# Performance work log

Hardware: AMD Instinct MI355X
Metric: run time of the kernel (lower is better)

The kernel has to match this reference:

```python
import jax, jax.numpy as jnp
import numpy as np

B, C, H, T = 256, 2048, 1024, 64  # batch, code_num, hidden_dim, max_len


def setup_inputs() -> dict:
    key = jax.random.key(0)
    ks = jax.random.split(key, 7)
    s_ih = 1.0 / np.sqrt(C)
    s_hh = 1.0 / np.sqrt(H)
    return {
        "noise": jax.random.normal(ks[0], (B, H), dtype=jnp.float32),
        "W_ih": jax.random.uniform(ks[1], (3 * H, C), jnp.float32, -s_ih, s_ih),
        "b_ih": jax.random.uniform(ks[2], (3 * H,), jnp.float32, -s_ih, s_ih),
        "W_hh": jax.random.uniform(ks[3], (3 * H, H), jnp.float32, -s_hh, s_hh),
        "b_hh": jax.random.uniform(ks[4], (3 * H,), jnp.float32, -s_hh, s_hh),
        "W_out": jax.random.uniform(ks[5], (C, H), jnp.float32, -s_hh, s_hh),
        "b_out": jax.random.uniform(ks[6], (C,), jnp.float32, -s_hh, s_hh),
        "max_len": T,
    }


def reference(noise, W_ih, b_ih, W_hh, b_hh, W_out, b_out, max_len):
    # initial codes = sigmoid(Linear(noise))
    codes0 = jax.nn.sigmoid(noise @ W_out.T + b_out)  # [B, C]
    h0 = jnp.zeros((noise.shape[0], W_hh.shape[1]), dtype=noise.dtype)  # [B, H]

    def step(carry, _):
        codes, h = carry
        gi = codes @ W_ih.T + b_ih           # [B, 3H]
        gh = h @ W_hh.T + b_hh               # [B, 3H]
        i_r, i_z, i_n = jnp.split(gi, 3, axis=-1)
        h_r, h_z, h_n = jnp.split(gh, 3, axis=-1)
        r = jax.nn.sigmoid(i_r + h_r)
        z = jax.nn.sigmoid(i_z + h_z)
        n = jnp.tanh(i_n + r * h_n)
        h_new = (1.0 - z) * n + z * h        # PyTorch GRUCell update
        logits = h_new @ W_out.T + b_out
        codes_new = jax.nn.sigmoid(logits)
        # sample at step t is codes BEFORE the cell; hidden is h AFTER
        return (codes_new, h_new), (codes, h_new)

    _, (samples, hiddens) = jax.lax.scan(step, (codes0, h0), None, length=max_len)
    samples = jnp.swapaxes(samples, 0, 1)  # [B, T, C]
    hiddens = jnp.swapaxes(hiddens, 0, 1)  # [B, T, H]
    return samples, hiddens
```

## Files before the change

### kernel.cpp

```cpp
#include <hip/hip_runtime.h>
#include <hip/hip_bf16.h>

#define BB 256
#define CC 2048
#define HD 1024
#define TT 64
#define H3 3072
#define NBLK 256
#define NGRP 8
#define GBLK 32
#define GROWS 32

typedef __attribute__((ext_vector_type(8)))  short bf16x8;
typedef __attribute__((ext_vector_type(4)))  float f32x4;
typedef __attribute__((ext_vector_type(16))) float f32x16;
typedef __attribute__((ext_vector_type(4)))  int   i32x4;

__device__ __forceinline__ float sigmoidf_(float x){ return 1.0f/(1.0f+__expf(-x)); }
__device__ __forceinline__ float tanhf_(float x){ float e=__expf(2.0f*x); return 1.0f - 2.0f/(e+1.0f); }
__device__ __forceinline__ unsigned short bfbits(float x){
  __hip_bfloat16 b = __float2bfloat16(x);
  return *reinterpret_cast<unsigned short*>(&b);
}
__device__ __forceinline__ void st_sys_bf16(__hip_bfloat16* p, float v){
  __hip_atomic_store((unsigned short*)p, bfbits(v), __ATOMIC_RELAXED, __HIP_MEMORY_SCOPE_SYSTEM);
}
__device__ __forceinline__ float ld_sys_bf16v(const __hip_bfloat16* p){
  unsigned short b = __hip_atomic_load((const unsigned short*)p, __ATOMIC_RELAXED, __HIP_MEMORY_SCOPE_SYSTEM);
  union { unsigned short u; __hip_bfloat16 h; } x; x.u = b;
  return __bfloat162float(x.h);
}
__device__ __forceinline__ i32x4 ld_sys16(const void* p){
  i32x4 r;
  asm volatile("global_load_dwordx4 %0, %1, off sc0 sc1"
               : "=v"(r) : "v"(p) : "memory");
  return r;
}
__device__ __forceinline__ void waitv0(){
  asm volatile("s_waitcnt vmcnt(0)" ::: "memory");
  __builtin_amdgcn_sched_barrier(0);
}
__device__ __forceinline__ void release_wb(){
  asm volatile("s_waitcnt vmcnt(0)\n\t"
               "buffer_wbl2 sc1\n\t"
               "s_waitcnt vmcnt(0)" ::: "memory");
}

__global__ void cvt_f32_bf16(const float* __restrict__ in, __hip_bfloat16* __restrict__ out, int n){
  int i = (blockIdx.x*blockDim.x + threadIdx.x)*4;
  int stride = gridDim.x*blockDim.x*4;
  for (; i < n; i += stride){
    float4 v = *reinterpret_cast<const float4*>(in + i);
    ushort4 s;
    s.x = bfbits(v.x); s.y = bfbits(v.y); s.z = bfbits(v.z); s.w = bfbits(v.w);
    *reinterpret_cast<ushort4*>(out + i) = s;
  }
}

#define MFMA32(a,b,c) __builtin_amdgcn_mfma_f32_32x32x16_bf16((a),(b),(c),0,0,0)

__global__ __launch_bounds__(1024, 4) void gru_persistent(
    const __hip_bfloat16* __restrict__ wih,
    const __hip_bfloat16* __restrict__ whh,
    const __hip_bfloat16* __restrict__ wout,
    const __hip_bfloat16* __restrict__ noise16,
    const float* __restrict__ bih,
    const float* __restrict__ bhh,
    const float* __restrict__ bout,
    float* __restrict__ samples,
    float* __restrict__ hiddens,
    __hip_bfloat16* cb0, __hip_bfloat16* cb1,
    __hip_bfloat16* hb0, __hip_bfloat16* hb1,
    unsigned* flagC, unsigned* flagH)
{
  __shared__ __align__(16) char actbuf[98304];
  __shared__ float ghbuf[3*4*256];

  const int tid  = threadIdx.x;
  const int lane = tid & 63;
  const int wid  = tid >> 6;
  const int g    = blockIdx.x >> 5;
  const int bsub = blockIdx.x & 31;
  const int lrow = lane & 31;
  const int lkg  = lane >> 5;

  auto signal = [&](unsigned* flags, unsigned gen){
    __syncthreads();
    if (tid == 0){
      release_wb();
      __hip_atomic_store(&flags[g*GBLK + bsub], gen, __ATOMIC_RELAXED, __HIP_MEMORY_SCOPE_SYSTEM);
    }
  };
  auto waitf = [&](unsigned* flags, unsigned gen){
    if (tid < GBLK){
      while (__hip_atomic_load(&flags[g*GBLK + tid], __ATOMIC_RELAXED, __HIP_MEMORY_SCOPE_SYSTEM) < gen)
        __builtin_amdgcn_s_sleep(2);
    }
    __syncthreads();
  };

  auto stage = [&](const __hip_bfloat16* src, int rowStride, int colBase){
    i32x4 r0, r1, r2, r3;
    {
      int s = tid;        int p = s>>6, l = s&63;
      r0 = ld_sys16(src + (size_t)(g*GROWS + (l&31))*rowStride + colBase + p*16 + (l>>5)*8);
    }{
      int s = tid+1024;   int p = s>>6, l = s&63;
      r1 = ld_sys16(src + (size_t)(g*GROWS + (l&31))*rowStride + colBase + p*16 + (l>>5)*8);
    }{
      int s = tid+2048;   int p = s>>6, l = s&63;
      r2 = ld_sys16(src + (size_t)(g*GROWS + (l&31))*rowStride + colBase + p*16 + (l>>5)*8);
    }{
      int s = tid+3072;   int p = s>>6, l = s&63;
      r3 = ld_sys16(src + (size_t)(g*GROWS + (l&31))*rowStride + colBase + p*16 + (l>>5)*8);
    }
    waitv0();
    { int s = tid;      *(i32x4*)(actbuf + (s>>6)*1024 + (s&63)*16) = r0; }
    { int s = tid+1024; *(i32x4*)(actbuf + (s>>6)*1024 + (s&63)*16) = r1; }
    { int s = tid+2048; *(i32x4*)(actbuf + (s>>6)*1024 + (s&63)*16) = r2; }
    { int s = tid+3072; *(i32x4*)(actbuf + (s>>6)*1024 + (s&63)*16) = r3; }
  };

  auto dumpAcc = [&](int slot, const f32x16& acc){
    char* base = actbuf + slot*4096 + lane*16;
#pragma unroll
    for (int q = 0; q < 4; q++){
      f32x4 v = { acc[q*4+0], acc[q*4+1], acc[q*4+2], acc[q*4+3] };
      *(f32x4*)(base + q*1024) = v;
    }
  };

  const f32x16 zacc = {0};

  auto phaseX = [&](const __hip_bfloat16* hsrc, __hip_bfloat16* codesDst, int t){
    stage(hsrc, HD, 0);
    __syncthreads();

    if (wid < 15){
      const int tile = wid / 3;
      const int ks   = wid % 3;
      const int fbeg = (ks == 0) ? 0 : (22 + 21*(ks-1));
      const int fend = (ks == 2) ? 64 : (22 + 21*ks);
      const __hip_bfloat16* wl;
      if (tile < 2) wl = wout + (size_t)(bsub*64 + tile*32 + lrow)*HD + lkg*8;
      else          wl = whh  + (size_t)((tile-2)*HD + bsub*32 + lrow)*HD + lkg*8;
      f32x16 acc = zacc;
#pragma unroll 8
      for (int f = fbeg; f < fend; f++){
        bf16x8 a = *(const bf16x8*)(actbuf + f*1024 + lane*16);
        bf16x8 b = *(const bf16x8*)(wl + f*16);
        acc = MFMA32(a, b, acc);
      }
      __syncthreads();
      dumpAcc(wid, acc);
    } else {
      __syncthreads();
    }
    __syncthreads();

    if (wid < 8){
      const int tile = wid >> 2, q = wid & 3;
      const int col  = bsub*64 + tile*32 + lrow;
      f32x4 s0 = *(const f32x4*)(actbuf + (tile*3+0)*4096 + q*1024 + lane*16);
      f32x4 s1 = *(const f32x4*)(actbuf + (tile*3+1)*4096 + q*1024 + lane*16);
      f32x4 s2 = *(const f32x4*)(actbuf + (tile*3+2)*4096 + q*1024 + lane*16);
      const float bo = bout[col];
#pragma unroll
      for (int j = 0; j < 4; j++){
        const int row  = j + 8*q + 4*lkg;
        const int brow = g*GROWS + row;
        float sv = sigmoidf_(s0[j] + s1[j] + s2[j] + bo);
        __builtin_nontemporal_store(sv, &samples[(size_t)brow*TT*CC + (size_t)t*CC + col]);
        st_sys_bf16(codesDst + (size_t)brow*CC + col, sv);
      }
    } else {
      for (int task = wid - 8; task < 12; task += 8){
        const int gt = task >> 2, q = task & 3;
        f32x4 r;
        if (t == 0){
          r = (f32x4){0.f,0.f,0.f,0.f};
        } else {
          f32x4 s0 = *(const f32x4*)(actbuf + ((2+gt)*3+0)*4096 + q*1024 + lane*16);
          f32x4 s1 = *(const f32x4*)(actbuf + ((2+gt)*3+1)*4096 + q*1024 + lane*16);
          f32x4 s2 = *(const f32x4*)(actbuf + ((2+gt)*3+2)*4096 + q*1024 + lane*16);
          r = (f32x4){ s0[0]+s1[0]+s2[0], s0[1]+s1[1]+s2[1],
                       s0[2]+s1[2]+s2[2], s0[3]+s1[3]+s2[3] };
        }
        *(f32x4*)&ghbuf[(gt*4+q)*256 + lane*4] = r;
      }
    }
  };

  auto phaseY = [&](const __hip_bfloat16* codesSrc, const __hip_bfloat16* hsrc,
                    __hip_bfloat16* hDst, int t){
    f32x16 acc = zacc;
    float hp[4]; float bI[3], bH[3];
    const int jcol = bsub*32 + lrow;

    stage(codesSrc, CC, 0);
    __syncthreads();
    if (wid < 12){
      const int gt = wid >> 2, ks = wid & 3;
      const __hip_bfloat16* wl = wih + (size_t)(gt*HD + bsub*32 + lrow)*CC + lkg*8;
#pragma unroll
      for (int i = 0; i < 16; i++){
        const int f = ks*16 + i;
        bf16x8 a = *(const bf16x8*)(actbuf + f*1024 + lane*16);
        bf16x8 b = *(const bf16x8*)(wl + f*16);
        acc = MFMA32(a, b, acc);
      }
    } else {
      const int q = wid - 12;
#pragma unroll
      for (int j = 0; j < 4; j++){
        const int row = j + 8*q + 4*lkg;
        hp[j] = (t == 0) ? 0.0f
              : ld_sys_bf16v(hsrc + (size_t)(g*GROWS + row)*HD + jcol);
      }
#pragma unroll
      for (int gt = 0; gt < 3; gt++){
        bI[gt] = bih[gt*HD + jcol];
        bH[gt] = bhh[gt*HD + jcol];
      }
    }
    __syncthreads();

    stage(codesSrc, CC, 1024);
    __syncthreads();
    if (wid < 12){
      const int gt = wid >> 2, ks = wid & 3;
      const __hip_bfloat16* wl = wih + (size_t)(gt*HD + bsub*32 + lrow)*CC + lkg*8;
#pragma unroll
      for (int i = 0; i < 16; i++){
        const int f = ks*16 + i;
        bf16x8 a = *(const bf16x8*)(actbuf + f*1024 + lane*16);
        bf16x8 b = *(const bf16x8*)(wl + 1024 + f*16);
        acc = MFMA32(a, b, acc);
      }
      __syncthreads();
      dumpAcc(wid, acc);
    } else {
      __syncthreads();
    }
    __syncthreads();

    if (wid >= 12){
      const int q = wid - 12;
      f32x4 gi[3], gh[3];
#pragma unroll
      for (int gt = 0; gt < 3; gt++){
        f32x4 s0 = *(const f32x4*)(actbuf + (gt*4+0)*4096 + q*1024 + lane*16);
        f32x4 s1 = *(const f32x4*)(actbuf + (gt*4+1)*4096 + q*1024 + lane*16);
        f32x4 s2 = *(const f32x4*)(actbuf + (gt*4+2)*4096 + q*1024 + lane*16);
        f32x4 s3 = *(const f32x4*)(actbuf + (gt*4+3)*4096 + q*1024 + lane*16);
        gi[gt] = (f32x4){ s0[0]+s1[0]+s2[0]+s3[0], s0[1]+s1[1]+s2[1]+s3[1],
                          s0[2]+s1[2]+s2[2]+s3[2], s0[3]+s1[3]+s2[3]+s3[3] };
        gh[gt] = *(const f32x4*)&ghbuf[(gt*4+q)*256 + lane*4];
      }
#pragma unroll
      for (int j = 0; j < 4; j++){
        const int row  = j + 8*q + 4*lkg;
        const int brow = g*GROWS + row;
        float r = sigmoidf_(gi[0][j] + gh[0][j] + bI[0] + bH[0]);
        float z = sigmoidf_(gi[1][j] + gh[1][j] + bI[1] + bH[1]);
        float n = tanhf_(gi[2][j] + bI[2] + r*(gh[2][j] + bH[2]));
        float hv = (1.0f - z)*n + z*hp[j];
        __builtin_nontemporal_store(hv, &hiddens[(size_t)brow*TT*HD + (size_t)t*HD + jcol]);
        st_sys_bf16(hDst + (size_t)brow*HD + jcol, hv);
      }
    }
  };

#pragma unroll 1
  for (int t = 0; t < TT; t++){
    const __hip_bfloat16* hcur = (t & 1) ? hb1 : hb0;
    __hip_bfloat16* codesCur   = (t & 1) ? cb1 : cb0;
    __hip_bfloat16* hnext      = (t & 1) ? hb0 : hb1;

    if (t > 0) waitf(flagH, (unsigned)t);
    phaseX((t == 0) ? noise16 : hcur, codesCur, t);
    signal(flagC, (unsigned)(t+1));

    waitf(flagC, (unsigned)(t+1));
    phaseY(codesCur, hcur, hnext, t);
    signal(flagH, (unsigned)(t+1));
  }
}

extern "C" void kernel_launch(void* const* d_in, const int* in_sizes, int n_in,
                              void* d_out, int out_size, void* d_ws, size_t ws_size,
                              hipStream_t stream) {
  const float* noise = (const float*)d_in[0];
  const float* W_ih  = (const float*)d_in[1];
  const float* b_ih  = (const float*)d_in[2];
  const float* W_hh  = (const float*)d_in[3];
  const float* b_hh  = (const float*)d_in[4];
  const float* W_out = (const float*)d_in[5];
  const float* b_out = (const float*)d_in[6];

  float* samples = (float*)d_out;
  float* hiddens = samples + (size_t)BB*TT*CC;

  char* w = (char*)d_ws;
  unsigned* flagC = (unsigned*)w;              w += 1024;
  unsigned* flagH = (unsigned*)w;              w += 1024;
  __hip_bfloat16* wih16 = (__hip_bfloat16*)w;  w += (size_t)H3*CC*2;
  __hip_bfloat16* whh16 = (__hip_bfloat16*)w;  w += (size_t)H3*HD*2;
  __hip_bfloat16* wout16= (__hip_bfloat16*)w;  w += (size_t)CC*HD*2;
  __hip_bfloat16* noise16=(__hip_bfloat16*)w;  w += (size_t)BB*HD*2;
  __hip_bfloat16* cb0   = (__hip_bfloat16*)w;  w += (size_t)BB*CC*2;
  __hip_bfloat16* cb1   = (__hip_bfloat16*)w;  w += (size_t)BB*CC*2;
  __hip_bfloat16* hb0   = (__hip_bfloat16*)w;  w += (size_t)BB*HD*2;
  __hip_bfloat16* hb1   = (__hip_bfloat16*)w;  w += (size_t)BB*HD*2;

  hipMemsetAsync(flagC, 0, 2048, stream);
  cvt_f32_bf16<<<2048, 256, 0, stream>>>(W_ih,  wih16,  H3*CC);
  cvt_f32_bf16<<<2048, 256, 0, stream>>>(W_hh,  whh16,  H3*HD);
  cvt_f32_bf16<<<1024, 256, 0, stream>>>(W_out, wout16, CC*HD);
  cvt_f32_bf16<<<256,  256, 0, stream>>>(noise, noise16, BB*HD);

  gru_persistent<<<NBLK, 1024, 0, stream>>>(
      wih16, whh16, wout16, noise16, b_ih, b_hh, b_out,
      samples, hiddens, cb0, cb1, hb0, hb1, flagC, flagH);
}
```

Measured before the change: 3.516 ms.

## Split persistent GRU across 512 blocks with 16-row groups and 16x16 MFMA

Doubles the persistent grid to 512 blocks, each owning 16 batch rows instead of 32, and switches from 32x32x16 to 16x16x32 bf16 MFMA tiles. Activations are staged in 512-column chunks through a double-buffered LDS buffer, with dedicated waves loading the next chunk while others compute. The previous hidden state is now kept in registers rather than reloaded from global memory. This cuts LDS use and per-block work to raise occupancy and parallelism, at the cost of more blocks in the flag-based cross-block barriers and reloading each weight tile for twice as many batch groups.

New measurement: 5.186 ms. +47.5%, slower.

```diff
diff --git a/kernel.cpp b/kernel.cpp
--- a/kernel.cpp
+++ b/kernel.cpp
@@ -6,14 +6,13 @@
 #define HD 1024
 #define TT 64
 #define H3 3072
-#define NBLK 256
-#define NGRP 8
+#define NBLK 512
+#define NGRP 16
 #define GBLK 32
-#define GROWS 32
+#define GROWS 16
 
 typedef __attribute__((ext_vector_type(8)))  short bf16x8;
 typedef __attribute__((ext_vector_type(4)))  float f32x4;
-typedef __attribute__((ext_vector_type(16))) float f32x16;
 typedef __attribute__((ext_vector_type(4)))  int   i32x4;
 
 __device__ __forceinline__ float sigmoidf_(float x){ return 1.0f/(1.0f+__expf(-x)); }
@@ -25,10 +24,8 @@
 __device__ __forceinline__ void st_sys_bf16(__hip_bfloat16* p, float v){
   __hip_atomic_store((unsigned short*)p, bfbits(v), __ATOMIC_RELAXED, __HIP_MEMORY_SCOPE_SYSTEM);
 }
-__device__ __forceinline__ float ld_sys_bf16v(const __hip_bfloat16* p){
-  unsigned short b = __hip_atomic_load((const unsigned short*)p, __ATOMIC_RELAXED, __HIP_MEMORY_SCOPE_SYSTEM);
-  union { unsigned short u; __hip_bfloat16 h; } x; x.u = b;
-  return __bfloat162float(x.h);
+__device__ __forceinline__ bf16x8 ldfrag(const __hip_bfloat16* p){
+  return *reinterpret_cast<const bf16x8*>(p);
 }
 __device__ __forceinline__ i32x4 ld_sys16(const void* p){
   i32x4 r;
@@ -57,9 +54,9 @@
   }
 }
 
-#define MFMA32(a,b,c) __builtin_amdgcn_mfma_f32_32x32x16_bf16((a),(b),(c),0,0,0)
-
-__global__ __launch_bounds__(1024, 4) void gru_persistent(
+#define MFMA16(a,b,c) __builtin_amdgcn_mfma_f32_16x16x32_bf16((a),(b),(c),0,0,0)
+
+__global__ __launch_bounds__(1024, 8) void gru_persistent(
     const __hip_bfloat16* __restrict__ wih,
     const __hip_bfloat16* __restrict__ whh,
     const __hip_bfloat16* __restrict__ wout,
@@ -73,16 +70,18 @@
     __hip_bfloat16* hb0, __hip_bfloat16* hb1,
     unsigned* flagC, unsigned* flagH)
 {
-  __shared__ __align__(16) char actbuf[98304];
-  __shared__ float ghbuf[3*4*256];
+  __shared__ __align__(16) char  chunkbuf[2][16384];
+  __shared__ __align__(16) float dumpbuf[12*64*4];
+  __shared__ __align__(16) float ghbuf[6*64*4];
 
   const int tid  = threadIdx.x;
   const int lane = tid & 63;
   const int wid  = tid >> 6;
-  const int g    = blockIdx.x >> 5;
-  const int bsub = blockIdx.x & 31;
-  const int lrow = lane & 31;
-  const int lkg  = lane >> 5;
+  const int bid  = blockIdx.x;
+  const int g    = bid >> 5;
+  const int bsub = bid & 31;
+  const int rl   = lane & 15;
+  const int kg   = lane >> 4;
 
   auto signal = [&](unsigned* flags, unsigned gen){
     __syncthreads();
@@ -99,172 +98,115 @@
     __syncthreads();
   };
 
-  auto stage = [&](const __hip_bfloat16* src, int rowStride, int colBase){
-    i32x4 r0, r1, r2, r3;
-    {
-      int s = tid;        int p = s>>6, l = s&63;
-      r0 = ld_sys16(src + (size_t)(g*GROWS + (l&31))*rowStride + colBase + p*16 + (l>>5)*8);
-    }{
-      int s = tid+1024;   int p = s>>6, l = s&63;
-      r1 = ld_sys16(src + (size_t)(g*GROWS + (l&31))*rowStride + colBase + p*16 + (l>>5)*8);
-    }{
-      int s = tid+2048;   int p = s>>6, l = s&63;
-      r2 = ld_sys16(src + (size_t)(g*GROWS + (l&31))*rowStride + colBase + p*16 + (l>>5)*8);
-    }{
-      int s = tid+3072;   int p = s>>6, l = s&63;
-      r3 = ld_sys16(src + (size_t)(g*GROWS + (l&31))*rowStride + colBase + p*16 + (l>>5)*8);
-    }
-    waitv0();
-    { int s = tid;      *(i32x4*)(actbuf + (s>>6)*1024 + (s&63)*16) = r0; }
-    { int s = tid+1024; *(i32x4*)(actbuf + (s>>6)*1024 + (s&63)*16) = r1; }
-    { int s = tid+2048; *(i32x4*)(actbuf + (s>>6)*1024 + (s&63)*16) = r2; }
-    { int s = tid+3072; *(i32x4*)(actbuf + (s>>6)*1024 + (s&63)*16) = r3; }
-  };
-
-  auto dumpAcc = [&](int slot, const f32x16& acc){
-    char* base = actbuf + slot*4096 + lane*16;
-#pragma unroll
-    for (int q = 0; q < 4; q++){
-      f32x4 v = { acc[q*4+0], acc[q*4+1], acc[q*4+2], acc[q*4+3] };
-      *(f32x4*)(base + q*1024) = v;
-    }
-  };
-
-  const f32x16 zacc = {0};
+  auto stageChunk = [&](const __hip_bfloat16* src, int RS, int kbase, int bufsel){
+    if (wid >= 12){
+      const int sw = wid - 12;
+      i32x4 r0, r1, r2, r3;
+      const __hip_bfloat16* base = src + (size_t)(g*GROWS + rl)*RS + kbase + kg*8;
+      r0 = ld_sys16(base + (sw*4+0)*32);
+      r1 = ld_sys16(base + (sw*4+1)*32);
+      r2 = ld_sys16(base + (sw*4+2)*32);
+      r3 = ld_sys16(base + (sw*4+3)*32);
+      waitv0();
+      char* b = chunkbuf[bufsel] + lane*16;
+      *(i32x4*)(b + (sw*4+0)*1024) = r0;
+      *(i32x4*)(b + (sw*4+1)*1024) = r1;
+      *(i32x4*)(b + (sw*4+2)*1024) = r2;
+      *(i32x4*)(b + (sw*4+3)*1024) = r3;
+    }
+  };
+
+  float hp[4] = {0.f, 0.f, 0.f, 0.f};
 
   auto phaseX = [&](const __hip_bfloat16* hsrc, __hip_bfloat16* codesDst, int t){
-    stage(hsrc, HD, 0);
-    __syncthreads();
-
-    if (wid < 15){
-      const int tile = wid / 3;
-      const int ks   = wid % 3;
-      const int fbeg = (ks == 0) ? 0 : (22 + 21*(ks-1));
-      const int fend = (ks == 2) ? 64 : (22 + 21*ks);
-      const __hip_bfloat16* wl;
-      if (tile < 2) wl = wout + (size_t)(bsub*64 + tile*32 + lrow)*HD + lkg*8;
-      else          wl = whh  + (size_t)((tile-2)*HD + bsub*32 + lrow)*HD + lkg*8;
-      f32x16 acc = zacc;
-#pragma unroll 8
-      for (int f = fbeg; f < fend; f++){
-        bf16x8 a = *(const bf16x8*)(actbuf + f*1024 + lane*16);
-        bf16x8 b = *(const bf16x8*)(wl + f*16);
-        acc = MFMA32(a, b, acc);
+    stageChunk(hsrc, HD, 0, 0);
+    __syncthreads();
+    f32x4 acc = {0.f,0.f,0.f,0.f};
+    const __hip_bfloat16* wl = nullptr;
+    if (wid < 4){
+      wl = wout + (size_t)(bsub*64 + wid*16 + rl)*HD + kg*8;
+    } else if (wid < 10){
+      const int gate = (wid-4) >> 1, ch = (wid-4) & 1;
+      wl = whh + (size_t)(gate*HD + bsub*32 + ch*16 + rl)*HD + kg*8;
+    }
+    const bool act = (wid < 4) || (wid < 10 && t > 0);
+#pragma unroll 1
+    for (int c = 0; c < 2; c++){
+      if (c == 0) stageChunk(hsrc, HD, 512, 1);
+      if (act){
+#pragma unroll
+        for (int p = 0; p < 16; p++){
+          bf16x8 a = *(const bf16x8*)(chunkbuf[c] + p*1024 + lane*16);
+          acc = MFMA16(a, ldfrag(wl + c*512 + p*32), acc);
+        }
       }
       __syncthreads();
-      dumpAcc(wid, acc);
-    } else {
-      __syncthreads();
-    }
-    __syncthreads();
-
-    if (wid < 8){
-      const int tile = wid >> 2, q = wid & 3;
-      const int col  = bsub*64 + tile*32 + lrow;
-      f32x4 s0 = *(const f32x4*)(actbuf + (tile*3+0)*4096 + q*1024 + lane*16);
-      f32x4 s1 = *(const f32x4*)(actbuf + (tile*3+1)*4096 + q*1024 + lane*16);
-      f32x4 s2 = *(const f32x4*)(actbuf + (tile*3+2)*4096 + q*1024 + lane*16);
+    }
+    if (wid < 4){
+      const int col = bsub*64 + wid*16 + rl;
       const float bo = bout[col];
 #pragma unroll
-      for (int j = 0; j < 4; j++){
-        const int row  = j + 8*q + 4*lkg;
-        const int brow = g*GROWS + row;
-        float sv = sigmoidf_(s0[j] + s1[j] + s2[j] + bo);
+      for (int q = 0; q < 4; q++){
+        const int brow = g*GROWS + kg*4 + q;
+        float sv = sigmoidf_(acc[q] + bo);
         __builtin_nontemporal_store(sv, &samples[(size_t)brow*TT*CC + (size_t)t*CC + col]);
         st_sys_bf16(codesDst + (size_t)brow*CC + col, sv);
       }
-    } else {
-      for (int task = wid - 8; task < 12; task += 8){
-        const int gt = task >> 2, q = task & 3;
-        f32x4 r;
-        if (t == 0){
-          r = (f32x4){0.f,0.f,0.f,0.f};
-        } else {
-          f32x4 s0 = *(const f32x4*)(actbuf + ((2+gt)*3+0)*4096 + q*1024 + lane*16);
-          f32x4 s1 = *(const f32x4*)(actbuf + ((2+gt)*3+1)*4096 + q*1024 + lane*16);
-          f32x4 s2 = *(const f32x4*)(actbuf + ((2+gt)*3+2)*4096 + q*1024 + lane*16);
-          r = (f32x4){ s0[0]+s1[0]+s2[0], s0[1]+s1[1]+s2[1],
-                       s0[2]+s1[2]+s2[2], s0[3]+s1[3]+s2[3] };
+    } else if (wid < 10){
+      f32x4 out = (t == 0) ? (f32x4){0.f,0.f,0.f,0.f} : acc;
+      *(f32x4*)&ghbuf[((wid-4)*64 + lane)*4] = out;
+    }
+  };
+
+  auto phaseY = [&](const __hip_bfloat16* codesSrc, __hip_bfloat16* hDst, int t){
+    stageChunk(codesSrc, CC, 0, 0);
+    __syncthreads();
+    f32x4 acc = {0.f,0.f,0.f,0.f};
+    const __hip_bfloat16* wl = nullptr;
+    int ks = 0;
+    if (wid < 12){
+      const int ct = wid >> 1;
+      ks = wid & 1;
+      const int gate = ct >> 1, ch = ct & 1;
+      wl = wih + (size_t)(gate*HD + bsub*32 + ch*16 + rl)*CC + kg*8;
+    }
+#pragma unroll 1
+    for (int c = 0; c < 4; c++){
+      if (c < 3) stageChunk(codesSrc, CC, (c+1)*512, (c+1)&1);
+      if (wid < 12 && (c >> 1) == ks){
+#pragma unroll
+        for (int p = 0; p < 16; p++){
+          bf16x8 a = *(const bf16x8*)(chunkbuf[c&1] + p*1024 + lane*16);
+          acc = MFMA16(a, ldfrag(wl + c*512 + p*32), acc);
         }
-        *(f32x4*)&ghbuf[(gt*4+q)*256 + lane*4] = r;
-      }
-    }
-  };
-
-  auto phaseY = [&](const __hip_bfloat16* codesSrc, const __hip_bfloat16* hsrc,
-                    __hip_bfloat16* hDst, int t){
-    f32x16 acc = zacc;
-    float hp[4]; float bI[3], bH[3];
-    const int jcol = bsub*32 + lrow;
-
-    stage(codesSrc, CC, 0);
-    __syncthreads();
-    if (wid < 12){
-      const int gt = wid >> 2, ks = wid & 3;
-      const __hip_bfloat16* wl = wih + (size_t)(gt*HD + bsub*32 + lrow)*CC + lkg*8;
-#pragma unroll
-      for (int i = 0; i < 16; i++){
-        const int f = ks*16 + i;
-        bf16x8 a = *(const bf16x8*)(actbuf + f*1024 + lane*16);
-        bf16x8 b = *(const bf16x8*)(wl + f*16);
-        acc = MFMA32(a, b, acc);
-      }
-    } else {
-      const int q = wid - 12;
-#pragma unroll
-      for (int j = 0; j < 4; j++){
-        const int row = j + 8*q + 4*lkg;
-        hp[j] = (t == 0) ? 0.0f
-              : ld_sys_bf16v(hsrc + (size_t)(g*GROWS + row)*HD + jcol);
-      }
-#pragma unroll
-      for (int gt = 0; gt < 3; gt++){
-        bI[gt] = bih[gt*HD + jcol];
-        bH[gt] = bhh[gt*HD + jcol];
-      }
-    }
-    __syncthreads();
-
-    stage(codesSrc, CC, 1024);
-    __syncthreads();
-    if (wid < 12){
-      const int gt = wid >> 2, ks = wid & 3;
-      const __hip_bfloat16* wl = wih + (size_t)(gt*HD + bsub*32 + lrow)*CC + lkg*8;
-#pragma unroll
-      for (int i = 0; i < 16; i++){
-        const int f = ks*16 + i;
-        bf16x8 a = *(const bf16x8*)(actbuf + f*1024 + lane*16);
-        bf16x8 b = *(const bf16x8*)(wl + 1024 + f*16);
-        acc = MFMA32(a, b, acc);
       }
       __syncthreads();
-      dumpAcc(wid, acc);
-    } else {
-      __syncthreads();
-    }
-    __syncthreads();
-
-    if (wid >= 12){
-      const int q = wid - 12;
+    }
+    if (wid < 12) *(f32x4*)&dumpbuf[(wid*64 + lane)*4] = acc;
+    __syncthreads();
+
+    if (wid == 12 || wid == 13){
+      const int ch   = wid - 12;
+      const int jcol = bsub*32 + ch*16 + rl;
+      const float bI0 = bih[jcol], bI1 = bih[jcol+HD], bI2 = bih[jcol+2*HD];
+      const float bH0 = bhh[jcol], bH1 = bhh[jcol+HD], bH2 = bhh[jcol+2*HD];
       f32x4 gi[3], gh[3];
 #pragma unroll
-      for (int gt = 0; gt < 3; gt++){
-        f32x4 s0 = *(const f32x4*)(actbuf + (gt*4+0)*4096 + q*1024 + lane*16);
-        f32x4 s1 = *(const f32x4*)(actbuf + (gt*4+1)*4096 + q*1024 + lane*16);
-        f32x4 s2 = *(const f32x4*)(actbuf + (gt*4+2)*4096 + q*1024 + lane*16);
-        f32x4 s3 = *(const f32x4*)(actbuf + (gt*4+3)*4096 + q*1024 + lane*16);
-        gi[gt] = (f32x4){ s0[0]+s1[0]+s2[0]+s3[0], s0[1]+s1[1]+s2[1]+s3[1],
-                          s0[2]+s1[2]+s2[2]+s3[2], s0[3]+s1[3]+s2[3]+s3[3] };
-        gh[gt] = *(const f32x4*)&ghbuf[(gt*4+q)*256 + lane*4];
-      }
-#pragma unroll
-      for (int j = 0; j < 4; j++){
-        const int row  = j + 8*q + 4*lkg;
-        const int brow = g*GROWS + row;
-        float r = sigmoidf_(gi[0][j] + gh[0][j] + bI[0] + bH[0]);
-        float z = sigmoidf_(gi[1][j] + gh[1][j] + bI[1] + bH[1]);
-        float n = tanhf_(gi[2][j] + bI[2] + r*(gh[2][j] + bH[2]));
-        float hv = (1.0f - z)*n + z*hp[j];
+      for (int gate = 0; gate < 3; gate++){
+        const int ct = gate*2 + ch;
+        f32x4 a0 = *(const f32x4*)&dumpbuf[((ct*2+0)*64 + lane)*4];
+        f32x4 a1 = *(const f32x4*)&dumpbuf[((ct*2+1)*64 + lane)*4];
+        gi[gate] = (f32x4){a0[0]+a1[0], a0[1]+a1[1], a0[2]+a1[2], a0[3]+a1[3]};
+        gh[gate] = *(const f32x4*)&ghbuf[((gate*2+ch)*64 + lane)*4];
+      }
+#pragma unroll
+      for (int q = 0; q < 4; q++){
+        const int brow = g*GROWS + kg*4 + q;
+        float r = sigmoidf_(gi[0][q] + gh[0][q] + bI0 + bH0);
+        float z = sigmoidf_(gi[1][q] + gh[1][q] + bI1 + bH1);
+        float n = tanhf_(gi[2][q] + bI2 + r*(gh[2][q] + bH2));
+        float hv = (1.0f - z)*n + z*hp[q];
+        hp[q] = hv;
         __builtin_nontemporal_store(hv, &hiddens[(size_t)brow*TT*HD + (size_t)t*HD + jcol]);
         st_sys_bf16(hDst + (size_t)brow*HD + jcol, hv);
       }
@@ -273,16 +215,16 @@
 
 #pragma unroll 1
   for (int t = 0; t < TT; t++){
-    const __hip_bfloat16* hcur = (t & 1) ? hb1 : hb0;
+    const __hip_bfloat16* hsrc = (t & 1) ? hb0 : hb1;
     __hip_bfloat16* codesCur   = (t & 1) ? cb1 : cb0;
-    __hip_bfloat16* hnext      = (t & 1) ? hb0 : hb1;
+    __hip_bfloat16* hDst       = (t & 1) ? hb1 : hb0;
 
     if (t > 0) waitf(flagH, (unsigned)t);
-    phaseX((t == 0) ? noise16 : hcur, codesCur, t);
+    phaseX((t == 0) ? noise16 : hsrc, codesCur, t);
     signal(flagC, (unsigned)(t+1));
 
     waitf(flagC, (unsigned)(t+1));
-    phaseY(codesCur, hcur, hnext, t);
+    phaseY(codesCur, hDst, t);
     signal(flagH, (unsigned)(t+1));
   }
 }
@@ -302,8 +244,8 @@
   float* hiddens = samples + (size_t)BB*TT*CC;
 
   char* w = (char*)d_ws;
-  unsigned* flagC = (unsigned*)w;              w += 1024;
-  unsigned* flagH = (unsigned*)w;              w += 1024;
+  unsigned* flagC = (unsigned*)w;              w += 2048;
+  unsigned* flagH = (unsigned*)w;              w += 2048;
   __hip_bfloat16* wih16 = (__hip_bfloat16*)w;  w += (size_t)H3*CC*2;
   __hip_bfloat16* whh16 = (__hip_bfloat16*)w;  w += (size_t)H3*HD*2;
   __hip_bfloat16* wout16= (__hip_bfloat16*)w;  w += (size_t)CC*HD*2;
@@ -313,7 +255,7 @@
   __hip_bfloat16* hb0   = (__hip_bfloat16*)w;  w += (size_t)BB*HD*2;
   __hip_bfloat16* hb1   = (__hip_bfloat16*)w;  w += (size_t)BB*HD*2;
 
-  hipMemsetAsync(flagC, 0, 2048, stream);
+  hipMemsetAsync(flagC, 0, 4096, stream);
   cvt_f32_bf16<<<2048, 256, 0, stream>>>(W_ih,  wih16,  H3*CC);
   cvt_f32_bf16<<<2048, 256, 0, stream>>>(W_hh,  whh16,  H3*HD);
   cvt_f32_bf16<<<1024, 256, 0, stream>>>(W_out, wout16, CC*HD);
```
